# Kernel optimization log

Hardware: AMD Instinct MI355X
Metric: run time of the kernel (lower is better)

## Reference

```python
import jax, jax.numpy as jnp
import numpy as np

D_VISION = 1024
D_BRANCH = 256
N_BRANCHES = 4
N_HEADS = 4
HEAD_DIM = D_BRANCH // N_HEADS
DIVERSITY_WEIGHT = 0.1
LN_EPS = 1e-5


def setup_inputs() -> dict:
    key = jax.random.key(0)
    ks = jax.random.split(key, 8)
    B, T, N = 8, 16, 256
    frame_patches = jax.random.normal(ks[0], (B, T, N, D_VISION), dtype=jnp.float32)
    # LayerNorm params (shared input_norm)
    ln_gamma = jnp.ones((D_VISION,), jnp.float32)
    ln_beta = jnp.zeros((D_VISION,), jnp.float32)
    # Per-branch params stacked on a leading branch dim
    query = jax.random.normal(ks[1], (N_BRANCHES, N_HEADS, HEAD_DIM), jnp.float32) * 0.02
    wstd = 1.0 / np.sqrt(D_VISION)
    Wk = jax.random.uniform(ks[2], (N_BRANCHES, D_VISION, D_BRANCH), jnp.float32, -wstd, wstd)
    bk = jax.random.uniform(ks[3], (N_BRANCHES, D_BRANCH), jnp.float32, -wstd, wstd)
    Wv = jax.random.uniform(ks[4], (N_BRANCHES, D_VISION, D_BRANCH), jnp.float32, -wstd, wstd)
    bv = jax.random.uniform(ks[5], (N_BRANCHES, D_BRANCH), jnp.float32, -wstd, wstd)
    ostd = 1.0 / np.sqrt(D_BRANCH)
    Wo = jax.random.uniform(ks[6], (N_BRANCHES, D_BRANCH, D_BRANCH), jnp.float32, -ostd, ostd)
    bo = jax.random.uniform(ks[7], (N_BRANCHES, D_BRANCH), jnp.float32, -ostd, ostd)
    return dict(frame_patches=frame_patches, ln_gamma=ln_gamma, ln_beta=ln_beta,
                query=query, Wk=Wk, bk=bk, Wv=Wv, bv=bv, Wo=Wo, bo=bo)


def _layernorm(x, g, b):
    mu = jnp.mean(x, axis=-1, keepdims=True)
    var = jnp.var(x, axis=-1, keepdims=True)
    return (x - mu) * jax.lax.rsqrt(var + LN_EPS) * g + b


def reference(frame_patches, ln_gamma, ln_beta, query, Wk, bk, Wv, bv, Wo, bo):
    B, T, N, D = frame_patches.shape
    nb, H, hd = query.shape
    db = H * hd
    scale = hd ** -0.5
    x = _layernorm(frame_patches.reshape(B * T, N, D), ln_gamma, ln_beta)  # (BT, N, D)
    # Batched k/v projections across all branches (the fusion opportunity)
    k = (jnp.einsum('bpd,ndk->nbpk', x, Wk) + bk[:, None, None, :]).reshape(nb, B * T, N, H, hd)
    v = (jnp.einsum('bpd,ndk->nbpk', x, Wv) + bv[:, None, None, :]).reshape(nb, B * T, N, H, hd)
    # Single learnable query per (branch, head) attends over patches
    scores = jnp.einsum('nbphd,nhd->nbhp', k, query) * scale  # (nb, BT, H, N)
    attn = jax.nn.softmax(scores, axis=-1)
    attn_avg = attn.mean(axis=2)  # (nb, BT, N) head-averaged, pre-dropout
    # Dropout is inference no-op (eval mode)
    pooled = jnp.einsum('nbhp,nbphd->nbhd', attn, v).reshape(nb, B * T, db)
    out = jnp.einsum('nbk,nkj->nbj', pooled, Wo) + bo[:, None, :]  # (nb, BT, db)
    streams = out.transpose(1, 0, 2).reshape(B, T, nb, db)
    # Diversity loss: mean pairwise cosine similarity of attention distributions
    norms = jnp.maximum(jnp.linalg.norm(attn_avg, axis=-1, keepdims=True), 1e-8)
    a = attn_avg / norms
    sims = jnp.einsum('ibn,jbn->ijb', a, a).mean(axis=-1)  # (nb, nb)
    mask = jnp.triu(jnp.ones((nb, nb), attn_avg.dtype), k=1)
    diversity_loss = DIVERSITY_WEIGHT * (sims * mask).sum() / mask.sum()
    return streams, diversity_loss
```

## Files before the change

### kernel.cpp

```cpp
#include <hip/hip_runtime.h>
#include <stdint.h>

#define BT      128
#define NPATCH  256
#define DV      1024
#define NB      4
#define DB      256
#define NH16    16
#define SCALE   0.125f
#define LNEPS   1e-5f

#define OFF_BWS    16384u
#define OFF_PSC    24608u
#define OFF_DRAW   25120u
#define OFF_STATS  549408u
#define OFF_W      614944u
#define OFF_CV     1139232u
#define OFF_DIV    1141280u
#define OFF_XBAR   1142048u
#define OFF_POOL   9530656u
#define XSLICE     2097152u

#define LROW 264

typedef short bf16x8 __attribute__((ext_vector_type(8)));
typedef float f32x4  __attribute__((ext_vector_type(4)));

__device__ __forceinline__ short f2bf(float f) {
    union { float f; unsigned u; } v; v.f = f;
    unsigned u = v.u;
    unsigned r = (u + 0x7fffu + ((u >> 16) & 1u)) >> 16;
    return (short)r;
}

__device__ __forceinline__ unsigned pk2(float lo, float hi) {
    union { float f; unsigned u; } a, b; a.f = lo; b.f = hi;
    return __builtin_amdgcn_perm(b.u, a.u, 0x07060302u);
}

__global__ __launch_bounds__(256) void kP(const float* __restrict__ Wk,
                                          const float* __restrict__ q,
                                          const float* __restrict__ g,
                                          const float* __restrict__ b,
                                          float* __restrict__ ws) {
    const int nh = blockIdx.x >> 4, ich = blockIdx.x & 15;
    const int n = nh >> 2, h = nh & 3;
    __shared__ float qs[64];
    __shared__ float redS[4], redC[4];
    const int t = threadIdx.x;
    if (t < 64) qs[t] = q[nh * 64 + t];
    __syncthreads();
    const int r = t >> 2, qd = t & 3;
    const int i = ich * 64 + r;
    const float* wrow = Wk + ((size_t)n * DV + i) * DB + h * 64 + qd * 16;
    float acc = 0.f;
    #pragma unroll
    for (int d = 0; d < 16; d += 4) {
        float4 w4 = *(const float4*)(wrow + d);
        acc += w4.x * qs[qd * 16 + d]     + w4.y * qs[qd * 16 + d + 1]
             + w4.z * qs[qd * 16 + d + 2] + w4.w * qs[qd * 16 + d + 3];
    }
    acc += __shfl_xor(acc, 1);
    acc += __shfl_xor(acc, 2);
    float gw = g[i] * acc;
    if (qd == 0) {
        unsigned short* bws = (unsigned short*)(ws + OFF_BWS);
        const int kt = i >> 5, oct = (r >> 3) & 3, j = r & 7;
        bws[((kt * 64 + oct * 16 + nh) << 3) + j] = (unsigned short)f2bf(gw);
    }
    float mS = (qd == 0) ? gw : 0.f;
    float mC = (qd == 0) ? b[i] * acc : 0.f;
    #pragma unroll
    for (int dd = 4; dd < 64; dd <<= 1) { mS += __shfl_xor(mS, dd); mC += __shfl_xor(mC, dd); }
    const int wave = t >> 6, lane = t & 63;
    if (lane == 0) { redS[wave] = mS; redC[wave] = mC; }
    __syncthreads();
    if (t == 0) {
        ws[OFF_PSC + (nh * 16 + ich) * 2 + 0] = redS[0] + redS[1] + redS[2] + redS[3];
        ws[OFF_PSC + (nh * 16 + ich) * 2 + 1] = redC[0] + redC[1] + redC[2] + redC[3];
    }
}

__global__ __launch_bounds__(256) void kA(const float* __restrict__ x,
                                          float* __restrict__ ws) {
    __shared__ unsigned short xs[64 * LROW];
    const int t = threadIdx.x;
    const int wv = t >> 6, lane = t & 63;
    const int m = lane & 15, oct = lane >> 4;
    const int row0 = blockIdx.x * 64;
    const bf16x8* bfp = (const bf16x8*)((const unsigned short*)(ws + OFF_BWS));
    const float* xb = x + (size_t)row0 * DV;

    float sum[16], sq[16];
    #pragma unroll
    for (int i = 0; i < 16; ++i) { sum[i] = 0.f; sq[i] = 0.f; }
    f32x4 acc = {0.f, 0.f, 0.f, 0.f};
    float4 r[16];

    auto loadr = [&](int c) {
        #pragma unroll
        for (int i = 0; i < 16; ++i)
            r[i] = *(const float4*)(xb + (size_t)(i * 4 + wv) * DV + c * 256 + lane * 4);
    };
    auto commit = [&]() {
        #pragma unroll
        for (int i = 0; i < 16; ++i) {
            float4 v = r[i];
            sum[i] += v.x + v.y + v.z + v.w;
            sq[i]  += v.x * v.x + v.y * v.y + v.z * v.z + v.w * v.w;
            uint2 pk; pk.x = pk2(v.x, v.y); pk.y = pk2(v.z, v.w);
            *(uint2*)&xs[(i * 4 + wv) * LROW + lane * 4] = pk;
        }
    };
    auto comp = [&](int c) {
        #pragma unroll
        for (int kt = 0; kt < 8; ++kt) {
            bf16x8 af = *(const bf16x8*)&xs[(wv * 16 + m) * LROW + kt * 32 + oct * 8];
            bf16x8 bf = bfp[(c * 8 + kt) * 64 + lane];
            acc = __builtin_amdgcn_mfma_f32_16x16x32_bf16(af, bf, acc, 0, 0, 0);
        }
    };

    loadr(0);
    for (int c = 0; c < 4; ++c) {
        __syncthreads();
        commit();
        __syncthreads();
        if (c < 3) loadr(c + 1);
        comp(c);
    }

    #pragma unroll
    for (int r2 = 0; r2 < 4; ++r2)
        ws[OFF_DRAW + (size_t)(row0 + wv * 16 + oct * 4 + r2) * 16 + m] = acc[r2];

    #pragma unroll
    for (int i = 0; i < 16; ++i) {
        float s = sum[i], q2 = sq[i];
        #pragma unroll
        for (int d = 1; d < 64; d <<= 1) { s += __shfl_xor(s, d); q2 += __shfl_xor(q2, d); }
        if (lane == 0) {
            const int row = row0 + i * 4 + wv;
            const float mu  = s * (1.f / 1024.f);
            const float var = q2 * (1.f / 1024.f) - mu * mu;
            float2 st; st.x = mu; st.y = rsqrtf(var + LNEPS);
            *(float2*)(ws + OFF_STATS + (size_t)row * 2) = st;
        }
    }
}

__global__ __launch_bounds__(256) void kB(const float* __restrict__ q,
                                          const float* __restrict__ bk,
                                          float* __restrict__ ws) {
    const int bt = blockIdx.x;
    const int t = threadIdx.x;
    __shared__ __attribute__((aligned(16))) float s_s[NH16 * NPATCH];
    __shared__ __attribute__((aligned(16))) float aavg[NB * NPATCH];
    __shared__ __attribute__((aligned(16))) float rstd_s[NPATCH];
    __shared__ __attribute__((aligned(16))) float mrs[NPATCH];
    __shared__ float Ss[NH16], Cbs[NH16];
    if (t < NH16) {
        const int nh2 = t, n2 = nh2 >> 2, h2 = nh2 & 3;
        float S = 0.f, C = 0.f;
        #pragma unroll
        for (int ich = 0; ich < 16; ++ich) {
            S += ws[OFF_PSC + (nh2 * 16 + ich) * 2 + 0];
            C += ws[OFF_PSC + (nh2 * 16 + ich) * 2 + 1];
        }
        float bkq = 0.f;
        #pragma unroll
        for (int d = 0; d < 64; ++d) bkq += bk[n2 * DB + h2 * 64 + d] * q[nh2 * 64 + d];
        Ss[t] = S; Cbs[t] = C + bkq;
    }
    const size_t row = (size_t)bt * NPATCH + t;
    const float2 st = *(const float2*)(ws + OFF_STATS + row * 2);
    const float mu = st.x, rstd = st.y;
    rstd_s[t] = rstd;
    mrs[t] = mu * rstd;
    __syncthreads();
    const float* dr = ws + OFF_DRAW + row * 16;
    #pragma unroll
    for (int nh = 0; nh < NH16; ++nh) {
        float D = dr[nh];
        s_s[nh * NPATCH + t] = (rstd * (D - mu * Ss[nh]) + Cbs[nh]) * SCALE;
    }
    __syncthreads();
    const int wave = t >> 6, lane = t & 63;
    for (int r = 0; r < 4; ++r) {
        const int nh = wave * 4 + r;
        float4 v = *(float4*)&s_s[nh * NPATCH + lane * 4];
        float mx = fmaxf(fmaxf(v.x, v.y), fmaxf(v.z, v.w));
        for (int d = 1; d < 64; d <<= 1) mx = fmaxf(mx, __shfl_xor(mx, d));
        float e0 = __expf(v.x - mx), e1 = __expf(v.y - mx);
        float e2 = __expf(v.z - mx), e3 = __expf(v.w - mx);
        float s = e0 + e1 + e2 + e3;
        for (int d = 1; d < 64; d <<= 1) s += __shfl_xor(s, d);
        float inv = 1.f / s;
        float4 a; a.x = e0 * inv; a.y = e1 * inv; a.z = e2 * inv; a.w = e3 * inv;
        *(float4*)&s_s[nh * NPATCH + lane * 4] = a;
        float4 r4 = *(float4*)&rstd_s[lane * 4];
        float4 wv; wv.x = a.x * r4.x; wv.y = a.y * r4.y; wv.z = a.z * r4.z; wv.w = a.w * r4.w;
        *(float4*)(ws + OFF_W + (size_t)(bt * NH16 + nh) * NPATCH + lane * 4) = wv;
    }
    __syncthreads();
    for (int r = 0; r < 4; ++r) {
        const int nh = wave * 4 + r;
        float4 a4 = *(float4*)&s_s[nh * NPATCH + lane * 4];
        float4 m4 = *(float4*)&mrs[lane * 4];
        float dd = a4.x * m4.x + a4.y * m4.y + a4.z * m4.z + a4.w * m4.w;
        for (int d = 1; d < 64; d <<= 1) dd += __shfl_xor(dd, d);
        if (lane == 0) ws[OFF_CV + bt * NH16 + nh] = dd;
    }
    #pragma unroll
    for (int n = 0; n < NB; ++n)
        aavg[n * NPATCH + t] = 0.25f * (s_s[(n * 4 + 0) * NPATCH + t] + s_s[(n * 4 + 1) * NPATCH + t]
                                      + s_s[(n * 4 + 2) * NPATCH + t] + s_s[(n * 4 + 3) * NPATCH + t]);
    __syncthreads();
    if (wave == 0) {
        float nrm[NB];
        #pragma unroll
        for (int n = 0; n < NB; ++n) {
            float4 v = *(float4*)&aavg[n * NPATCH + lane * 4];
            float ss = v.x * v.x + v.y * v.y + v.z * v.z + v.w * v.w;
            for (int d = 1; d < 64; d <<= 1) ss += __shfl_xor(ss, d);
            nrm[n] = fmaxf(sqrtf(ss), 1e-8f);
        }
        int pi = 0;
        for (int i = 0; i < NB; ++i)
            for (int j = i + 1; j < NB; ++j) {
                float4 va = *(float4*)&aavg[i * NPATCH + lane * 4];
                float4 vb = *(float4*)&aavg[j * NPATCH + lane * 4];
                float dd = va.x * vb.x + va.y * vb.y + va.z * vb.z + va.w * vb.w;
                for (int d = 1; d < 64; d <<= 1) dd += __shfl_xor(dd, d);
                if (lane == 0) ws[OFF_DIV + bt * 6 + pi] = dd / (nrm[i] * nrm[j]);
                ++pi;
            }
    }
}

__global__ __launch_bounds__(256) void kC(const float* __restrict__ x,
                                          float* __restrict__ ws) {
    const int bt = blockIdx.x;
    const int qq = blockIdx.y;
    const int t = threadIdx.x;
    __shared__ __attribute__((aligned(16))) float w_s[64 * 16];
    for (int idx = t; idx < 1024; idx += 256) {
        int p = idx >> 4, nh = idx & 15;
        w_s[idx] = ws[OFF_W + (size_t)(bt * NH16 + nh) * NPATCH + qq * 64 + p];
    }
    float4 acc[16];
    #pragma unroll
    for (int i = 0; i < 16; ++i) { acc[i].x = 0.f; acc[i].y = 0.f; acc[i].z = 0.f; acc[i].w = 0.f; }
    __syncthreads();
    const float* xp = x + (size_t)(bt * NPATCH + qq * 64) * DV + t * 4;
    #define FMA4(k, wgt, xv) acc[k].x += (wgt) * xv.x; acc[k].y += (wgt) * xv.y; \
                             acc[k].z += (wgt) * xv.z; acc[k].w += (wgt) * xv.w;
    #define PBLOCK(p, xv) { \
        float4 a0 = *(const float4*)&w_s[(p) * 16 + 0]; \
        float4 a1 = *(const float4*)&w_s[(p) * 16 + 4]; \
        float4 a2 = *(const float4*)&w_s[(p) * 16 + 8]; \
        float4 a3 = *(const float4*)&w_s[(p) * 16 + 12]; \
        FMA4(0, a0.x, xv)  FMA4(1, a0.y, xv)  FMA4(2, a0.z, xv)  FMA4(3, a0.w, xv) \
        FMA4(4, a1.x, xv)  FMA4(5, a1.y, xv)  FMA4(6, a1.z, xv)  FMA4(7, a1.w, xv) \
        FMA4(8, a2.x, xv)  FMA4(9, a2.y, xv)  FMA4(10, a2.z, xv) FMA4(11, a2.w, xv) \
        FMA4(12, a3.x, xv) FMA4(13, a3.y, xv) FMA4(14, a3.z, xv) FMA4(15, a3.w, xv) }
    for (int p = 0; p < 16; ++p) {
        float4 xv0 = *(const float4*)(xp + (size_t)(p +  0) * DV);
        float4 xv1 = *(const float4*)(xp + (size_t)(p + 16) * DV);
        float4 xv2 = *(const float4*)(xp + (size_t)(p + 32) * DV);
        float4 xv3 = *(const float4*)(xp + (size_t)(p + 48) * DV);
        PBLOCK(p, xv0)
        PBLOCK(p + 16, xv1)
        PBLOCK(p + 32, xv2)
        PBLOCK(p + 48, xv3)
    }
    #undef PBLOCK
    #undef FMA4
    #pragma unroll
    for (int nh = 0; nh < 16; ++nh)
        *(float4*)(ws + OFF_XBAR + (size_t)qq * XSLICE
                   + ((size_t)bt * NH16 + nh) * DV + t * 4) = acc[nh];
}

__global__ __launch_bounds__(256) void kD1(const float* __restrict__ Wv,
                                           const float* __restrict__ g,
                                           const float* __restrict__ b,
                                           const float* __restrict__ bv,
                                           float* __restrict__ ws) {
    const int nh = blockIdx.x & 15, btg = blockIdx.x >> 4;
    const int n = nh >> 2, h = nh & 3;
    const int bt0 = btg * 8, cb = h * 64;
    __shared__ __attribute__((aligned(16))) float xs[8][1024];
    __shared__ __attribute__((aligned(16))) float gs[1024], bs[1024];
    __shared__ float red[4][64][10];
    const int t = threadIdx.x;
    for (int e = t; e < 2048; e += 256) {
        const int bt = e >> 8, i4 = e & 255;
        const size_t b0 = OFF_XBAR + ((size_t)(bt0 + bt) * NH16 + nh) * DV + i4 * 4;
        float4 s = {0.f, 0.f, 0.f, 0.f};
        #pragma unroll
        for (int qq = 0; qq < 4; ++qq) {
            float4 v = *(const float4*)(ws + b0 + (size_t)qq * XSLICE);
            s.x += v.x; s.y += v.y; s.z += v.z; s.w += v.w;
        }
        *(float4*)&xs[bt][i4 * 4] = s;
    }
    for (int e = t; e < 1024; e += 256) { gs[e] = g[e]; bs[e] = b[e]; }
    __syncthreads();
    const int c = t & 63, sub = t >> 6;
    float acc[8];
    #pragma unroll
    for (int l = 0; l < 8; ++l) acc[l] = 0.f;
    float gv = 0.f, bvv = 0.f;
    const float* wvp = Wv + ((size_t)n * DV + sub * 256) * DB + cb + c;
    const int ib0 = sub * 256;
    #pragma unroll 2
    for (int gidx = 0; gidx < 64; ++gidx) {
        const int ib = ib0 + gidx * 4;
        float w0 = wvp[(size_t)(gidx * 4 + 0) * DB];
        float w1 = wvp[(size_t)(gidx * 4 + 1) * DB];
        float w2 = wvp[(size_t)(gidx * 4 + 2) * DB];
        float w3 = wvp[(size_t)(gidx * 4 + 3) * DB];
        float4 g4 = *(const float4*)&gs[ib];
        float4 b4 = *(const float4*)&bs[ib];
        float q0 = g4.x * w0, q1 = g4.y * w1, q2 = g4.z * w2, q3 = g4.w * w3;
        gv  += q0 + q1 + q2 + q3;
        bvv += b4.x * w0 + b4.y * w1 + b4.z * w2 + b4.w * w3;
        #pragma unroll
        for (int l = 0; l < 8; ++l) {
            float4 xr = *(const float4*)&xs[l][ib];
            acc[l] += xr.x * q0 + xr.y * q1 + xr.z * q2 + xr.w * q3;
        }
    }
    #pragma unroll
    for (int l = 0; l < 8; ++l) red[sub][c][l] = acc[l];
    red[sub][c][8] = gv; red[sub][c][9] = bvv;
    __syncthreads();
    const int c2 = t & 63, l0 = t >> 6;
    float gvS = red[0][c2][8] + red[1][c2][8] + red[2][c2][8] + red[3][c2][8];
    float bvS = red[0][c2][9] + red[1][c2][9] + red[2][c2][9] + red[3][c2][9];
    float base = bv[n * DB + cb + c2] + bvS;
    #pragma unroll
    for (int li = 0; li < 2; ++li) {
        const int l = l0 + li * 4;
        float p = red[0][c2][l] + red[1][c2][l] + red[2][c2][l] + red[3][c2][l];
        float C = ws[OFF_CV + (bt0 + l) * NH16 + nh];
        ws[OFF_POOL + ((size_t)n * BT + bt0 + l) * DB + cb + c2] = p - C * gvS + base;
    }
}

__global__ __launch_bounds__(256) void kD2(const float* __restrict__ Wo,
                                           const float* __restrict__ bo,
                                           const float* __restrict__ ws,
                                           float* __restrict__ out) {
    const int btg = blockIdx.x & 15, jq = (blockIdx.x >> 4) & 3, n = blockIdx.x >> 6;
    const int bt0 = btg * 8, j0 = jq * 64;
    __shared__ __attribute__((aligned(16))) float ps[8][256];
    __shared__ float red[4][64][8];
    __shared__ float dred[4];
    const int t = threadIdx.x;
    for (int e = t; e < 512; e += 256) {
        const int bt = e >> 6, c4 = e & 63;
        *(float4*)&ps[bt][c4 * 4] =
            *(const float4*)(ws + OFF_POOL + ((size_t)n * BT + bt0 + bt) * DB + c4 * 4);
    }
    float dacc = 0.f;
    if (blockIdx.x == 0)
        for (int idx = t; idx < 768; idx += 256) dacc += ws[OFF_DIV + idx];
    for (int d = 1; d < 64; d <<= 1) dacc += __shfl_xor(dacc, d);
    if ((t & 63) == 0) dred[t >> 6] = dacc;
    __syncthreads();
    if (blockIdx.x == 0 && t == 0)
        out[131072] = 0.1f * (dred[0] + dred[1] + dred[2] + dred[3]) / 768.f;
    const int j = t & 63, sub = t >> 6;
    float acc[8];
    #pragma unroll
    for (int l = 0; l < 8; ++l) acc[l] = 0.f;
    const float* wop = Wo + ((size_t)n * DB + sub * 64) * DB + j0 + j;
    const int cb0 = sub * 64;
    #pragma unroll 2
    for (int gidx = 0; gidx < 16; ++gidx) {
        const int cb = cb0 + gidx * 4;
        float w0 = wop[(size_t)(gidx * 4 + 0) * DB];
        float w1 = wop[(size_t)(gidx * 4 + 1) * DB];
        float w2 = wop[(size_t)(gidx * 4 + 2) * DB];
        float w3 = wop[(size_t)(gidx * 4 + 3) * DB];
        #pragma unroll
        for (int l = 0; l < 8; ++l) {
            float4 pr = *(const float4*)&ps[l][cb];
            acc[l] += pr.x * w0 + pr.y * w1 + pr.z * w2 + pr.w * w3;
        }
    }
    #pragma unroll
    for (int l = 0; l < 8; ++l) red[sub][j][l] = acc[l];
    __syncthreads();
    const int j2 = t & 63, l0 = t >> 6;
    float bov = bo[n * DB + j0 + j2];
    #pragma unroll
    for (int li = 0; li < 2; ++li) {
        const int l = l0 + li * 4;
        float o = red[0][j2][l] + red[1][j2][l] + red[2][j2][l] + red[3][j2][l] + bov;
        out[((size_t)(bt0 + l) * NB + n) * DB + j0 + j2] = o;
    }
}

extern "C" void kernel_launch(void* const* d_in, const int* in_sizes, int n_in,
                              void* d_out, int out_size, void* d_ws, size_t ws_size,
                              hipStream_t stream) {
    const float* x  = (const float*)d_in[0];
    const float* g  = (const float*)d_in[1];
    const float* b  = (const float*)d_in[2];
    const float* q  = (const float*)d_in[3];
    const float* Wk = (const float*)d_in[4];
    const float* bk = (const float*)d_in[5];
    const float* Wv = (const float*)d_in[6];
    const float* bv = (const float*)d_in[7];
    const float* Wo = (const float*)d_in[8];
    const float* bo = (const float*)d_in[9];
    float* out = (float*)d_out;
    float* ws  = (float*)d_ws;

    hipLaunchKernelGGL(kP,  dim3(256),    dim3(256), 0, stream, Wk, q, g, b, ws);
    hipLaunchKernelGGL(kA,  dim3(512),    dim3(256), 0, stream, x, ws);
    hipLaunchKernelGGL(kB,  dim3(128),    dim3(256), 0, stream, q, bk, ws);
    hipLaunchKernelGGL(kC,  dim3(128, 4), dim3(256), 0, stream, x, ws);
    hipLaunchKernelGGL(kD1, dim3(256),    dim3(256), 0, stream, Wv, g, b, bv, ws);
    hipLaunchKernelGGL(kD2, dim3(256),    dim3(256), 0, stream, Wo, bo, ws, out);
}
```

Baseline: 290.1 us.

## Fuse softmax kernel into pooling kernel and split kD1 across more blocks

The softmax/attention kernel kB is merged into kC. Each of the four qq blocks per bt now recomputes the scores and softmax in LDS and builds its weight tile directly, which removes the OFF_W global round trip and one launch. Only qq==0 writes the CV and diversity outputs. The S/C setup reduction is parallelised across all threads with shuffles, and kD1 is retiled to 4 rows per block over 512 blocks to raise parallelism. In exchange, the softmax work is done four times redundantly and Wv is re-read more often in kD1.

```diff
diff --git a/kernel.cpp b/kernel.cpp
--- a/kernel.cpp
+++ b/kernel.cpp
@@ -149,42 +149,44 @@
     }
 }
 
-__global__ __launch_bounds__(256) void kB(const float* __restrict__ q,
+__global__ __launch_bounds__(256) void kC(const float* __restrict__ x,
+                                          const float* __restrict__ q,
                                           const float* __restrict__ bk,
                                           float* __restrict__ ws) {
     const int bt = blockIdx.x;
+    const int qq = blockIdx.y;
     const int t = threadIdx.x;
     __shared__ __attribute__((aligned(16))) float s_s[NH16 * NPATCH];
     __shared__ __attribute__((aligned(16))) float aavg[NB * NPATCH];
+    __shared__ __attribute__((aligned(16))) float w_s[64 * 16];
     __shared__ __attribute__((aligned(16))) float rstd_s[NPATCH];
     __shared__ __attribute__((aligned(16))) float mrs[NPATCH];
     __shared__ float Ss[NH16], Cbs[NH16];
-    if (t < NH16) {
-        const int nh2 = t, n2 = nh2 >> 2, h2 = nh2 & 3;
-        float S = 0.f, C = 0.f;
-        #pragma unroll
-        for (int ich = 0; ich < 16; ++ich) {
-            S += ws[OFF_PSC + (nh2 * 16 + ich) * 2 + 0];
-            C += ws[OFF_PSC + (nh2 * 16 + ich) * 2 + 1];
-        }
-        float bkq = 0.f;
-        #pragma unroll
-        for (int d = 0; d < 64; ++d) bkq += bk[n2 * DB + h2 * 64 + d] * q[nh2 * 64 + d];
-        Ss[t] = S; Cbs[t] = C + bkq;
+
+    {
+        const int nh = t >> 4, ich = t & 15;
+        float S = ws[OFF_PSC + t * 2 + 0];
+        float C = ws[OFF_PSC + t * 2 + 1];
+        const int n2 = nh >> 2, h2 = nh & 3;
+        const float* bkp = bk + n2 * DB + h2 * 64 + ich * 4;
+        const float* qp  = q + nh * 64 + ich * 4;
+        C += bkp[0] * qp[0] + bkp[1] * qp[1] + bkp[2] * qp[2] + bkp[3] * qp[3];
+        #pragma unroll
+        for (int d = 1; d < 16; d <<= 1) { S += __shfl_xor(S, d); C += __shfl_xor(C, d); }
+        if (ich == 0) { Ss[nh] = S; Cbs[nh] = C; }
     }
     const size_t row = (size_t)bt * NPATCH + t;
     const float2 st = *(const float2*)(ws + OFF_STATS + row * 2);
-    const float mu = st.x, rstd = st.y;
-    rstd_s[t] = rstd;
-    mrs[t] = mu * rstd;
-    __syncthreads();
+    rstd_s[t] = st.y;
+    mrs[t] = st.x * st.y;
+    __syncthreads();
+
     const float* dr = ws + OFF_DRAW + row * 16;
     #pragma unroll
-    for (int nh = 0; nh < NH16; ++nh) {
-        float D = dr[nh];
-        s_s[nh * NPATCH + t] = (rstd * (D - mu * Ss[nh]) + Cbs[nh]) * SCALE;
-    }
-    __syncthreads();
+    for (int nh = 0; nh < NH16; ++nh)
+        s_s[nh * NPATCH + t] = (st.y * (dr[nh] - st.x * Ss[nh]) + Cbs[nh]) * SCALE;
+    __syncthreads();
+
     const int wave = t >> 6, lane = t & 63;
     for (int r = 0; r < 4; ++r) {
         const int nh = wave * 4 + r;
@@ -198,60 +200,54 @@
         float inv = 1.f / s;
         float4 a; a.x = e0 * inv; a.y = e1 * inv; a.z = e2 * inv; a.w = e3 * inv;
         *(float4*)&s_s[nh * NPATCH + lane * 4] = a;
-        float4 r4 = *(float4*)&rstd_s[lane * 4];
-        float4 wv; wv.x = a.x * r4.x; wv.y = a.y * r4.y; wv.z = a.z * r4.z; wv.w = a.w * r4.w;
-        *(float4*)(ws + OFF_W + (size_t)(bt * NH16 + nh) * NPATCH + lane * 4) = wv;
-    }
-    __syncthreads();
-    for (int r = 0; r < 4; ++r) {
-        const int nh = wave * 4 + r;
-        float4 a4 = *(float4*)&s_s[nh * NPATCH + lane * 4];
-        float4 m4 = *(float4*)&mrs[lane * 4];
-        float dd = a4.x * m4.x + a4.y * m4.y + a4.z * m4.z + a4.w * m4.w;
-        for (int d = 1; d < 64; d <<= 1) dd += __shfl_xor(dd, d);
-        if (lane == 0) ws[OFF_CV + bt * NH16 + nh] = dd;
-    }
-    #pragma unroll
-    for (int n = 0; n < NB; ++n)
-        aavg[n * NPATCH + t] = 0.25f * (s_s[(n * 4 + 0) * NPATCH + t] + s_s[(n * 4 + 1) * NPATCH + t]
-                                      + s_s[(n * 4 + 2) * NPATCH + t] + s_s[(n * 4 + 3) * NPATCH + t]);
-    __syncthreads();
-    if (wave == 0) {
-        float nrm[NB];
-        #pragma unroll
-        for (int n = 0; n < NB; ++n) {
-            float4 v = *(float4*)&aavg[n * NPATCH + lane * 4];
-            float ss = v.x * v.x + v.y * v.y + v.z * v.z + v.w * v.w;
-            for (int d = 1; d < 64; d <<= 1) ss += __shfl_xor(ss, d);
-            nrm[n] = fmaxf(sqrtf(ss), 1e-8f);
-        }
-        int pi = 0;
-        for (int i = 0; i < NB; ++i)
-            for (int j = i + 1; j < NB; ++j) {
-                float4 va = *(float4*)&aavg[i * NPATCH + lane * 4];
-                float4 vb = *(float4*)&aavg[j * NPATCH + lane * 4];
-                float dd = va.x * vb.x + va.y * vb.y + va.z * vb.z + va.w * vb.w;
-                for (int d = 1; d < 64; d <<= 1) dd += __shfl_xor(dd, d);
-                if (lane == 0) ws[OFF_DIV + bt * 6 + pi] = dd / (nrm[i] * nrm[j]);
-                ++pi;
+    }
+    __syncthreads();
+
+    if (qq == 0) {
+        for (int r = 0; r < 4; ++r) {
+            const int nh = wave * 4 + r;
+            float4 a4 = *(float4*)&s_s[nh * NPATCH + lane * 4];
+            float4 m4 = *(float4*)&mrs[lane * 4];
+            float dd = a4.x * m4.x + a4.y * m4.y + a4.z * m4.z + a4.w * m4.w;
+            for (int d = 1; d < 64; d <<= 1) dd += __shfl_xor(dd, d);
+            if (lane == 0) ws[OFF_CV + bt * NH16 + nh] = dd;
+        }
+        #pragma unroll
+        for (int nb2 = 0; nb2 < NB; ++nb2)
+            aavg[nb2 * NPATCH + t] = 0.25f * (s_s[(nb2 * 4 + 0) * NPATCH + t] + s_s[(nb2 * 4 + 1) * NPATCH + t]
+                                            + s_s[(nb2 * 4 + 2) * NPATCH + t] + s_s[(nb2 * 4 + 3) * NPATCH + t]);
+        __syncthreads();
+        if (wave == 0) {
+            float nrm[NB];
+            #pragma unroll
+            for (int nb2 = 0; nb2 < NB; ++nb2) {
+                float4 v = *(float4*)&aavg[nb2 * NPATCH + lane * 4];
+                float ss = v.x * v.x + v.y * v.y + v.z * v.z + v.w * v.w;
+                for (int d = 1; d < 64; d <<= 1) ss += __shfl_xor(ss, d);
+                nrm[nb2] = fmaxf(sqrtf(ss), 1e-8f);
             }
-    }
-}
-
-__global__ __launch_bounds__(256) void kC(const float* __restrict__ x,
-                                          float* __restrict__ ws) {
-    const int bt = blockIdx.x;
-    const int qq = blockIdx.y;
-    const int t = threadIdx.x;
-    __shared__ __attribute__((aligned(16))) float w_s[64 * 16];
+            int pi = 0;
+            for (int i2 = 0; i2 < NB; ++i2)
+                for (int j2 = i2 + 1; j2 < NB; ++j2) {
+                    float4 va = *(float4*)&aavg[i2 * NPATCH + lane * 4];
+                    float4 vb = *(float4*)&aavg[j2 * NPATCH + lane * 4];
+                    float dd = va.x * vb.x + va.y * vb.y + va.z * vb.z + va.w * vb.w;
+                    for (int d = 1; d < 64; d <<= 1) dd += __shfl_xor(dd, d);
+                    if (lane == 0) ws[OFF_DIV + bt * 6 + pi] = dd / (nrm[i2] * nrm[j2]);
+                    ++pi;
+                }
+        }
+    }
+
     for (int idx = t; idx < 1024; idx += 256) {
-        int p = idx >> 4, nh = idx & 15;
-        w_s[idx] = ws[OFF_W + (size_t)(bt * NH16 + nh) * NPATCH + qq * 64 + p];
-    }
+        const int p = idx >> 4, nh = idx & 15;
+        w_s[idx] = s_s[nh * NPATCH + qq * 64 + p] * rstd_s[qq * 64 + p];
+    }
+    __syncthreads();
+
     float4 acc[16];
     #pragma unroll
     for (int i = 0; i < 16; ++i) { acc[i].x = 0.f; acc[i].y = 0.f; acc[i].z = 0.f; acc[i].w = 0.f; }
-    __syncthreads();
     const float* xp = x + (size_t)(bt * NPATCH + qq * 64) * DV + t * 4;
     #define FMA4(k, wgt, xv) acc[k].x += (wgt) * xv.x; acc[k].y += (wgt) * xv.y; \
                              acc[k].z += (wgt) * xv.z; acc[k].w += (wgt) * xv.w;
@@ -289,12 +285,12 @@
                                            float* __restrict__ ws) {
     const int nh = blockIdx.x & 15, btg = blockIdx.x >> 4;
     const int n = nh >> 2, h = nh & 3;
-    const int bt0 = btg * 8, cb = h * 64;
-    __shared__ __attribute__((aligned(16))) float xs[8][1024];
+    const int bt0 = btg * 4, cb = h * 64;
+    __shared__ __attribute__((aligned(16))) float xs[4][1024];
     __shared__ __attribute__((aligned(16))) float gs[1024], bs[1024];
-    __shared__ float red[4][64][10];
+    __shared__ float red[4][64][6];
     const int t = threadIdx.x;
-    for (int e = t; e < 2048; e += 256) {
+    for (int e = t; e < 1024; e += 256) {
         const int bt = e >> 8, i4 = e & 255;
         const size_t b0 = OFF_XBAR + ((size_t)(bt0 + bt) * NH16 + nh) * DV + i4 * 4;
         float4 s = {0.f, 0.f, 0.f, 0.f};
@@ -308,9 +304,9 @@
     for (int e = t; e < 1024; e += 256) { gs[e] = g[e]; bs[e] = b[e]; }
     __syncthreads();
     const int c = t & 63, sub = t >> 6;
-    float acc[8];
-    #pragma unroll
-    for (int l = 0; l < 8; ++l) acc[l] = 0.f;
+    float acc[4];
+    #pragma unroll
+    for (int l = 0; l < 4; ++l) acc[l] = 0.f;
     float gv = 0.f, bvv = 0.f;
     const float* wvp = Wv + ((size_t)n * DV + sub * 256) * DB + cb + c;
     const int ib0 = sub * 256;
@@ -327,26 +323,22 @@
         gv  += q0 + q1 + q2 + q3;
         bvv += b4.x * w0 + b4.y * w1 + b4.z * w2 + b4.w * w3;
         #pragma unroll
-        for (int l = 0; l < 8; ++l) {
+        for (int l = 0; l < 4; ++l) {
             float4 xr = *(const float4*)&xs[l][ib];
             acc[l] += xr.x * q0 + xr.y * q1 + xr.z * q2 + xr.w * q3;
         }
     }
     #pragma unroll
-    for (int l = 0; l < 8; ++l) red[sub][c][l] = acc[l];
-    red[sub][c][8] = gv; red[sub][c][9] = bvv;
-    __syncthreads();
-    const int c2 = t & 63, l0 = t >> 6;
-    float gvS = red[0][c2][8] + red[1][c2][8] + red[2][c2][8] + red[3][c2][8];
-    float bvS = red[0][c2][9] + red[1][c2][9] + red[2][c2][9] + red[3][c2][9];
+    for (int l = 0; l < 4; ++l) red[sub][c][l] = acc[l];
+    red[sub][c][4] = gv; red[sub][c][5] = bvv;
+    __syncthreads();
+    const int c2 = t & 63, l = t >> 6;
+    float gvS = red[0][c2][4] + red[1][c2][4] + red[2][c2][4] + red[3][c2][4];
+    float bvS = red[0][c2][5] + red[1][c2][5] + red[2][c2][5] + red[3][c2][5];
     float base = bv[n * DB + cb + c2] + bvS;
-    #pragma unroll
-    for (int li = 0; li < 2; ++li) {
-        const int l = l0 + li * 4;
-        float p = red[0][c2][l] + red[1][c2][l] + red[2][c2][l] + red[3][c2][l];
-        float C = ws[OFF_CV + (bt0 + l) * NH16 + nh];
-        ws[OFF_POOL + ((size_t)n * BT + bt0 + l) * DB + cb + c2] = p - C * gvS + base;
-    }
+    float p = red[0][c2][l] + red[1][c2][l] + red[2][c2][l] + red[3][c2][l];
+    float C = ws[OFF_CV + (bt0 + l) * NH16 + nh];
+    ws[OFF_POOL + ((size_t)n * BT + bt0 + l) * DB + cb + c2] = p - C * gvS + base;
 }
 
 __global__ __launch_bounds__(256) void kD2(const float* __restrict__ Wo,
@@ -422,8 +414,7 @@
 
     hipLaunchKernelGGL(kP,  dim3(256),    dim3(256), 0, stream, Wk, q, g, b, ws);
     hipLaunchKernelGGL(kA,  dim3(512),    dim3(256), 0, stream, x, ws);
-    hipLaunchKernelGGL(kB,  dim3(128),    dim3(256), 0, stream, q, bk, ws);
-    hipLaunchKernelGGL(kC,  dim3(128, 4), dim3(256), 0, stream, x, ws);
-    hipLaunchKernelGGL(kD1, dim3(256),    dim3(256), 0, stream, Wv, g, b, bv, ws);
+    hipLaunchKernelGGL(kC,  dim3(128, 4), dim3(256), 0, stream, x, q, bk, ws);
+    hipLaunchKernelGGL(kD1, dim3(512),    dim3(256), 0, stream, Wv, g, b, bv, ws);
     hipLaunchKernelGGL(kD2, dim3(256),    dim3(256), 0, stream, Wo, bo, ws, out);
 }
```

New measurement: 281.0 us. -3.1%, faster.
